# Kernel optimization log

Measured on AMD Instinct MI355X. Metric: run time of the kernel, lower is better.

## Reference

```python
import jax, jax.numpy as jnp
import numpy as np

CHANNELS = 96


def make_sharpen_kernel(channels: int) -> jnp.ndarray:
    # (C_out, C_in, 3, 3), block-diagonal: per-channel 3x3 sharpen stencil
    k = jnp.full((3, 3), -0.1, dtype=jnp.float32).at[1, 1].set(1.8)
    eye = jnp.eye(channels, dtype=jnp.float32)  # (C, C)
    return eye[:, :, None, None] * k[None, None, :, :]


def setup_inputs() -> dict:
    key = jax.random.key(0)
    x = jax.random.normal(key, (16, CHANNELS, 256, 256), dtype=jnp.float32)
    kernel = make_sharpen_kernel(CHANNELS)
    return {"x": x, "kernel": kernel}


def reference(x, kernel):
    # Faithful to F.conv2d(x, kernel, stride=1, padding=1) with the dense
    # (block-diagonal) kernel the torch module constructs.
    return jax.lax.conv_general_dilated(
        x, kernel,
        window_strides=(1, 1),
        padding=((1, 1), (1, 1)),
        dimension_numbers=("NCHW", "OIHW", "NCHW"),
    )
```

## Files before the change

### kernel.cpp

```cpp
#include <hip/hip_runtime.h>

#define CHN 96
#define IMG_H 256
#define IMG_W 256
#define STRIP 64
#define WPB 8
#define GRP 4
#define NG (STRIP / GRP)

typedef float vfloat4 __attribute__((ext_vector_type(4)));

__device__ __forceinline__ vfloat4 ldrow(const float* xp, int yy, int col) {
    if (yy < IMG_H)
        return __builtin_nontemporal_load(
            (const vfloat4*)(xp + (size_t)yy * IMG_W + col));
    return (vfloat4){0.f, 0.f, 0.f, 0.f};
}

__device__ __forceinline__ vfloat4 hsum3(vfloat4 v, int lane) {
    float l = __shfl_up(v.w, 1);
    float r = __shfl_down(v.x, 1);
    if (lane == 0)  l = 0.f;
    if (lane == 63) r = 0.f;
    float t1 = v.x + v.y;
    float t2 = v.z + v.w;
    vfloat4 h;
    h.x = l  + t1;
    h.y = t1 + v.z;
    h.z = v.y + t2;
    h.w = t2 + r;
    return h;
}

__device__ __forceinline__ void compute_group(const vfloat4* buf,
                                              vfloat4& hprev, vfloat4& hcur,
                                              vfloat4& ccur,
                                              float wn, float wd,
                                              float* op, int y, int col, int lane) {
    #pragma unroll
    for (int j = 0; j < GRP; ++j) {
        vfloat4 hn = hsum3(buf[j], lane);
        vfloat4 s  = hprev + hcur + hn;
        vfloat4 o  = s * wn + ccur * wd;
        __builtin_nontemporal_store(
            o, (vfloat4*)(op + (size_t)(y + j) * IMG_W + col));
        hprev = hcur;
        hcur  = hn;
        ccur  = buf[j];
    }
}

__global__ __launch_bounds__(WPB * 64, 6)
void sharpen3x3_lean(const float* __restrict__ x,
                     const float* __restrict__ kern,
                     float* __restrict__ out)
{
    const int lane = threadIdx.x & 63;
    const int wave = threadIdx.x >> 6;

    const int strip_id = blockIdx.x * WPB + wave;
    const int spp      = IMG_H / STRIP;
    const int plane    = strip_id / spp;
    const int sy       = (strip_id % spp) * STRIP;
    const int c        = plane % CHN;

    const float* kw = kern + ((size_t)c * CHN + c) * 9;
    const float wn = kw[0];
    const float wd = kw[4] - wn;

    const float* xp = x   + (size_t)plane * IMG_H * IMG_W;
    float*       op = out + (size_t)plane * IMG_H * IMG_W;
    const int col = 4 * lane;

    vfloat4 A[GRP], B[GRP];
    #pragma unroll
    for (int j = 0; j < GRP; ++j) A[j] = ldrow(xp, sy + 1 + j, col);

    vfloat4 hprev, hcur, ccur;
    if (sy == 0) {
        hprev = (vfloat4){0.f, 0.f, 0.f, 0.f};
    } else {
        hprev = hsum3(*(const vfloat4*)(xp + (size_t)(sy - 1) * IMG_W + col), lane);
    }
    {
        vfloat4 v0 = *(const vfloat4*)(xp + (size_t)sy * IMG_W + col);
        hcur = hsum3(v0, lane);
        ccur = v0;
    }

    #pragma unroll 1
    for (int g = 0; g < NG; g += 2) {
        const int y = sy + g * GRP;

        #pragma unroll
        for (int j = 0; j < GRP; ++j) B[j] = ldrow(xp, y + GRP + 1 + j, col);
        compute_group(A, hprev, hcur, ccur, wn, wd, op, y, col, lane);

        if (g + 2 < NG) {
            #pragma unroll
            for (int j = 0; j < GRP; ++j) A[j] = ldrow(xp, y + 2 * GRP + 1 + j, col);
        }
        compute_group(B, hprev, hcur, ccur, wn, wd, op, y + GRP, col, lane);
    }
}

extern "C" void kernel_launch(void* const* d_in, const int* in_sizes, int n_in,
                              void* d_out, int out_size, void* d_ws, size_t ws_size,
                              hipStream_t stream) {
    const float* x    = (const float*)d_in[0];
    const float* kern = (const float*)d_in[1];
    float* out        = (float*)d_out;

    const int n_strips = 16 * CHN * (IMG_H / STRIP);
    const int grid     = n_strips / WPB;

    hipLaunchKernelGGL(sharpen3x3_lean, dim3(grid), dim3(WPB * 64),
                       0, stream, x, kern, out);
}
```

Baseline: 162.6 us.

## Shorten per-wave strips and fully unroll for more thread-level parallelism

Cuts each wave's strip from 64 to 16 rows and blocks from 8 to 4 waves, and raises the launch-bounds occupancy hint. The grid gets larger and the latency-bound row loop is fully unrolled, so more independent waves hide memory latency. Input loads switch from nontemporal to normal cached loads, so the halo rows shared between adjacent strips can hit in cache. The cost is more redundant halo reads per strip, from 66/64 to 18/16 rows, plus extra block launches.

```diff
diff --git a/kernel.cpp b/kernel.cpp
--- a/kernel.cpp
+++ b/kernel.cpp
@@ -3,8 +3,8 @@
 #define CHN 96
 #define IMG_H 256
 #define IMG_W 256
-#define STRIP 64
-#define WPB 8
+#define STRIP 16
+#define WPB 4
 #define GRP 4
 #define NG (STRIP / GRP)
 
@@ -12,8 +12,7 @@
 
 __device__ __forceinline__ vfloat4 ldrow(const float* xp, int yy, int col) {
     if (yy < IMG_H)
-        return __builtin_nontemporal_load(
-            (const vfloat4*)(xp + (size_t)yy * IMG_W + col));
+        return *(const vfloat4*)(xp + (size_t)yy * IMG_W + col);
     return (vfloat4){0.f, 0.f, 0.f, 0.f};
 }
 
@@ -25,35 +24,17 @@
     float t1 = v.x + v.y;
     float t2 = v.z + v.w;
     vfloat4 h;
-    h.x = l  + t1;
-    h.y = t1 + v.z;
+    h.x = l   + t1;
+    h.y = t1  + v.z;
     h.z = v.y + t2;
-    h.w = t2 + r;
+    h.w = t2  + r;
     return h;
 }
 
-__device__ __forceinline__ void compute_group(const vfloat4* buf,
-                                              vfloat4& hprev, vfloat4& hcur,
-                                              vfloat4& ccur,
-                                              float wn, float wd,
-                                              float* op, int y, int col, int lane) {
-    #pragma unroll
-    for (int j = 0; j < GRP; ++j) {
-        vfloat4 hn = hsum3(buf[j], lane);
-        vfloat4 s  = hprev + hcur + hn;
-        vfloat4 o  = s * wn + ccur * wd;
-        __builtin_nontemporal_store(
-            o, (vfloat4*)(op + (size_t)(y + j) * IMG_W + col));
-        hprev = hcur;
-        hcur  = hn;
-        ccur  = buf[j];
-    }
-}
-
-__global__ __launch_bounds__(WPB * 64, 6)
-void sharpen3x3_lean(const float* __restrict__ x,
-                     const float* __restrict__ kern,
-                     float* __restrict__ out)
+__global__ __launch_bounds__(WPB * 64, 8)
+void sharpen3x3_tlp(const float* __restrict__ x,
+                    const float* __restrict__ kern,
+                    float* __restrict__ out)
 {
     const int lane = threadIdx.x & 63;
     const int wave = threadIdx.x >> 6;
@@ -72,9 +53,9 @@
     float*       op = out + (size_t)plane * IMG_H * IMG_W;
     const int col = 4 * lane;
 
-    vfloat4 A[GRP], B[GRP];
+    vfloat4 buf[2][GRP];
     #pragma unroll
-    for (int j = 0; j < GRP; ++j) A[j] = ldrow(xp, sy + 1 + j, col);
+    for (int j = 0; j < GRP; ++j) buf[0][j] = ldrow(xp, sy + 1 + j, col);
 
     vfloat4 hprev, hcur, ccur;
     if (sy == 0) {
@@ -88,19 +69,25 @@
         ccur = v0;
     }
 
-    #pragma unroll 1
-    for (int g = 0; g < NG; g += 2) {
-        const int y = sy + g * GRP;
-
+    #pragma unroll
+    for (int g = 0; g < NG; ++g) {
+        if (g + 1 < NG) {
+            #pragma unroll
+            for (int j = 0; j < GRP; ++j)
+                buf[(g + 1) & 1][j] = ldrow(xp, sy + (g + 1) * GRP + 1 + j, col);
+        }
         #pragma unroll
-        for (int j = 0; j < GRP; ++j) B[j] = ldrow(xp, y + GRP + 1 + j, col);
-        compute_group(A, hprev, hcur, ccur, wn, wd, op, y, col, lane);
-
-        if (g + 2 < NG) {
-            #pragma unroll
-            for (int j = 0; j < GRP; ++j) A[j] = ldrow(xp, y + 2 * GRP + 1 + j, col);
+        for (int j = 0; j < GRP; ++j) {
+            const int y = sy + g * GRP + j;
+            vfloat4 hn = hsum3(buf[g & 1][j], lane);
+            vfloat4 s  = hprev + hcur + hn;
+            vfloat4 o  = s * wn + ccur * wd;
+            __builtin_nontemporal_store(
+                o, (vfloat4*)(op + (size_t)y * IMG_W + col));
+            hprev = hcur;
+            hcur  = hn;
+            ccur  = buf[g & 1][j];
         }
-        compute_group(B, hprev, hcur, ccur, wn, wd, op, y + GRP, col, lane);
     }
 }
 
@@ -114,6 +101,6 @@
     const int n_strips = 16 * CHN * (IMG_H / STRIP);
     const int grid     = n_strips / WPB;
 
-    hipLaunchKernelGGL(sharpen3x3_lean, dim3(grid), dim3(WPB * 64),
+    hipLaunchKernelGGL(sharpen3x3_tlp, dim3(grid), dim3(WPB * 64),
                        0, stream, x, kern, out);
 }
```

Result: slower. 270.4 us (+66.3%).
